# Optimization experiments

Hardware: AMD Instinct MI355X
Metric: run time of the kernel (lower is better)

Reference implementation:

```python
import jax, jax.numpy as jnp
import numpy as np

SCALING = 32.0 / 16.0  # alpha / rank


def setup_inputs() -> dict:
    key = jax.random.key(0)
    k1, k2, k3, k4, k5 = jax.random.split(key, 5)
    B_, S, D_in, D_out, R = 4, 2048, 4096, 4096, 16
    x = jax.random.normal(k1, (B_, S, D_in), dtype=jnp.float32)
    W = jax.random.normal(k2, (D_out, D_in), dtype=jnp.float32) * (1.0 / np.sqrt(D_in))
    b = jax.random.normal(k3, (D_out,), dtype=jnp.float32) * 0.02
    lora_A = jax.random.normal(k4, (R, D_in), dtype=jnp.float32) * (1.0 / np.sqrt(D_in))
    lora_B = jax.random.normal(k5, (D_out, R), dtype=jnp.float32) * 0.02
    return {"x": x, "W": W, "b": b, "lora_A": lora_A, "lora_B": lora_B}


def reference(x, W, b, lora_A, lora_B):
    # Base linear: y = x @ W^T + b
    base = jnp.einsum('bsd,od->bso', x, W) + b
    # LoRA path: ((x @ A^T) @ B^T) * scaling  (dropout=0 -> identity)
    xa = jnp.einsum('bsd,rd->bsr', x, lora_A)      # [B,S,r]
    lora = jnp.einsum('bsr,or->bso', xa, lora_B)    # [B,S,D_out]
    return base + lora * SCALING
```

## Files before the change

### kernel.cpp

```cpp
#include <hip/hip_runtime.h>
#include <hip/hip_bf16.h>
#include <stdint.h>

typedef __bf16 bf16x8 __attribute__((ext_vector_type(8)));
typedef float  f32x4  __attribute__((ext_vector_type(4)));
typedef unsigned short u16x8 __attribute__((ext_vector_type(8)));


__device__ __forceinline__ unsigned short f32_to_bf16_rne(float f) {
  union { float f; unsigned int u; } v; v.f = f;
  unsigned int u = v.u;
  unsigned int r = u + 0x7fffu + ((u >> 16) & 1u);
  return (unsigned short)(r >> 16);
}

__device__ __forceinline__ void async16(const unsigned short* g, unsigned short* l) {
  __builtin_amdgcn_global_load_lds(
      (const __attribute__((address_space(1))) unsigned int*)g,
      (__attribute__((address_space(3))) unsigned int*)l,
      16, 0, 0);
}

__global__ __launch_bounds__(256) void make_wp(const float* __restrict__ W,
                                               const float* __restrict__ lA,
                                               const float* __restrict__ lB,
                                               unsigned short* __restrict__ Wp) {
  const int o   = blockIdx.x;
  const int tid = threadIdx.x;
  __shared__ float sB[16];
  if (tid < 16) sB[tid] = lB[o * 16 + tid] * 2.0f;
  __syncthreads();
  #pragma unroll
  for (int it = 0; it < 4; ++it) {
    const int k = (it * 256 + tid) * 4;
    float4 acc = *(const float4*)(W + (size_t)o * 4096 + k);
    #pragma unroll
    for (int r = 0; r < 16; ++r) {
      const float4 a = *(const float4*)(lA + (size_t)r * 4096 + k);
      const float s = sB[r];
      acc.x += s * a.x; acc.y += s * a.y; acc.z += s * a.z; acc.w += s * a.w;
    }
    ushort4 ov;
    ov.x = f32_to_bf16_rne(acc.x);
    ov.y = f32_to_bf16_rne(acc.y);
    ov.z = f32_to_bf16_rne(acc.z);
    ov.w = f32_to_bf16_rne(acc.w);
    *(ushort4*)(Wp + (size_t)o * 4096 + k) = ov;
  }
}

__global__ __launch_bounds__(256) void cast_x(const float* __restrict__ x,
                                              unsigned short* __restrict__ xb,
                                              int n8) {
  const int idx = blockIdx.x * 256 + threadIdx.x;
  if (idx >= n8) return;
  const float4* p = (const float4*)x + (size_t)idx * 2;
  const float4 f0 = p[0], f1 = p[1];
  u16x8 o;
  o[0] = f32_to_bf16_rne(f0.x); o[1] = f32_to_bf16_rne(f0.y);
  o[2] = f32_to_bf16_rne(f0.z); o[3] = f32_to_bf16_rne(f0.w);
  o[4] = f32_to_bf16_rne(f1.x); o[5] = f32_to_bf16_rne(f1.y);
  o[6] = f32_to_bf16_rne(f1.z); o[7] = f32_to_bf16_rne(f1.w);
  *((u16x8*)xb + idx) = o;
}

#define BM 128
#define BN 128
#define BK 32
#define GEMM_M 8192
#define GEMM_N 4096
#define GEMM_K 4096

template <bool A_F32>
__global__ __launch_bounds__(256) void gemm_bias(
    const void* __restrict__ Aptr,
    const unsigned short* __restrict__ B,
    const float* __restrict__ bias,
    float* __restrict__ C) {
  __shared__ __align__(16) unsigned short sA[BM * BK];
  __shared__ __align__(16) unsigned short sB[BM * BK];

  const int tid  = threadIdx.x;
  const int wave = tid >> 6;
  const int lane = tid & 63;

  const int srow = tid >> 2;
  const int scol = (tid & 3) << 3;

  const size_t a_row0 = (size_t)blockIdx.y * BM;
  const size_t b_row0 = (size_t)blockIdx.x * BN;

  const unsigned short* bg0 = B + (b_row0 +      srow) * GEMM_K + scol;
  const unsigned short* bg1 = B + (b_row0 + 64 + srow) * GEMM_K + scol;

  unsigned short* sA0 = sA +        wave * 512;
  unsigned short* sA1 = sA + 2048 + wave * 512;
  unsigned short* sB0 = sB +        wave * 512;
  unsigned short* sB1 = sB + 2048 + wave * 512;

  const unsigned short* ag0 = nullptr; const unsigned short* ag1 = nullptr;
  const float* af0 = nullptr; const float* af1 = nullptr;
  if constexpr (A_F32) {
    af0 = (const float*)Aptr + (a_row0 +      srow) * GEMM_K + scol;
    af1 = (const float*)Aptr + (a_row0 + 64 + srow) * GEMM_K + scol;
  } else {
    ag0 = (const unsigned short*)Aptr + (a_row0 +      srow) * GEMM_K + scol;
    ag1 = (const unsigned short*)Aptr + (a_row0 + 64 + srow) * GEMM_K + scol;
  }
  unsigned short* sAw0 = sA +        tid * 8;
  unsigned short* sAw1 = sA + 2048 + tid * 8;

  const int wm   = (wave >> 1) * 64;
  const int wn   = (wave & 1) * 64;
  const int lrow = lane & 15;
  const int lk   = (lane >> 4) * 8;

  const unsigned short* sa_rd = sA + (wm + lrow) * BK + lk;
  const unsigned short* sb_rd = sB + (wn + lrow) * BK + lk;

  f32x4 acc[4][4];
  #pragma unroll
  for (int i = 0; i < 4; ++i)
    #pragma unroll
    for (int j = 0; j < 4; ++j)
      acc[i][j] = (f32x4){0.f, 0.f, 0.f, 0.f};

  for (int k0 = 0; k0 < GEMM_K; k0 += BK) {
    __syncthreads();
    async16(bg0 + k0, sB0);
    async16(bg1 + k0, sB1);
    if constexpr (A_F32) {
      const float* p0 = af0 + k0;
      const float* p1 = af1 + k0;
      const float4 x0 = *(const float4*)(p0);
      const float4 x1 = *(const float4*)(p0 + 4);
      const float4 y0 = *(const float4*)(p1);
      const float4 y1 = *(const float4*)(p1 + 4);
      u16x8 w0, w1;
      w0[0] = f32_to_bf16_rne(x0.x); w0[1] = f32_to_bf16_rne(x0.y);
      w0[2] = f32_to_bf16_rne(x0.z); w0[3] = f32_to_bf16_rne(x0.w);
      w0[4] = f32_to_bf16_rne(x1.x); w0[5] = f32_to_bf16_rne(x1.y);
      w0[6] = f32_to_bf16_rne(x1.z); w0[7] = f32_to_bf16_rne(x1.w);
      w1[0] = f32_to_bf16_rne(y0.x); w1[1] = f32_to_bf16_rne(y0.y);
      w1[2] = f32_to_bf16_rne(y0.z); w1[3] = f32_to_bf16_rne(y0.w);
      w1[4] = f32_to_bf16_rne(y1.x); w1[5] = f32_to_bf16_rne(y1.y);
      w1[6] = f32_to_bf16_rne(y1.z); w1[7] = f32_to_bf16_rne(y1.w);
      *(u16x8*)sAw0 = w0;
      *(u16x8*)sAw1 = w1;
    } else {
      async16(ag0 + k0, sA0);
      async16(ag1 + k0, sA1);
    }
    __syncthreads();

    bf16x8 af[4], bf[4];
    #pragma unroll
    for (int i = 0; i < 4; ++i) {
      af[i] = *(const bf16x8*)(sa_rd + i * 16 * BK);
      bf[i] = *(const bf16x8*)(sb_rd + i * 16 * BK);
    }
    #pragma unroll
    for (int i = 0; i < 4; ++i)
      #pragma unroll
      for (int j = 0; j < 4; ++j)
        acc[i][j] = __builtin_amdgcn_mfma_f32_16x16x32_bf16(af[i], bf[j], acc[i][j], 0, 0, 0);
  }

  const int row0 = (int)a_row0 + wm + (lane >> 4) * 4;
  const int col0 = (int)b_row0 + wn + lrow;
  float bv[4];
  #pragma unroll
  for (int j = 0; j < 4; ++j) bv[j] = bias[col0 + j * 16];
  #pragma unroll
  for (int i = 0; i < 4; ++i)
    #pragma unroll
    for (int j = 0; j < 4; ++j) {
      const int col = col0 + j * 16;
      #pragma unroll
      for (int r = 0; r < 4; ++r) {
        const int row = row0 + i * 16 + r;
        C[(size_t)row * GEMM_N + col] = acc[i][j][r] + bv[j];
      }
    }
}


extern "C" void kernel_launch(void* const* d_in, const int* in_sizes, int n_in,
                              void* d_out, int out_size, void* d_ws, size_t ws_size,
                              hipStream_t stream) {
  const float* x  = (const float*)d_in[0];
  const float* W  = (const float*)d_in[1];
  const float* b  = (const float*)d_in[2];
  const float* lA = (const float*)d_in[3];
  const float* lB = (const float*)d_in[4];
  float* out = (float*)d_out;
  (void)in_sizes; (void)n_in; (void)out_size;

  const size_t WP_BYTES = (size_t)4096 * 4096 * 2;
  const size_t XB_BYTES = (size_t)8192 * 4096 * 2;
  unsigned short* Wp = (unsigned short*)d_ws;

  make_wp<<<4096, 256, 0, stream>>>(W, lA, lB, Wp);

  if (ws_size >= WP_BYTES + XB_BYTES) {
    unsigned short* xb = Wp + (size_t)4096 * 4096;
    cast_x<<<(4194304 + 255) / 256, 256, 0, stream>>>(x, xb, 4194304);
    gemm_bias<false><<<dim3(GEMM_N / BN, GEMM_M / BM), 256, 0, stream>>>(
        (const void*)xb, Wp, b, out);
  } else {
    gemm_bias<true><<<dim3(GEMM_N / BN, GEMM_M / BM), 256, 0, stream>>>(
        (const void*)x, Wp, b, out);
  }
}
```

Baseline: 602.1 us.

## Fuse x bf16 cast into GEMM and reuse LoRA A across rows in make_wp

```diff
diff --git a/kernel.cpp b/kernel.cpp
--- a/kernel.cpp
+++ b/kernel.cpp
@@ -25,20 +25,23 @@
                                                const float* __restrict__ lA,
                                                const float* __restrict__ lB,
                                                unsigned short* __restrict__ Wp) {
-  const int o   = blockIdx.x;
-  const int tid = threadIdx.x;
-  __shared__ float sB[16];
-  if (tid < 16) sB[tid] = lB[o * 16 + tid] * 2.0f;
-  __syncthreads();
+  const int ro = (blockIdx.x & 511) * 8;
+  const int k  = (blockIdx.x >> 9) * 1024 + threadIdx.x * 4;
+
+  float4 a[16];
   #pragma unroll
-  for (int it = 0; it < 4; ++it) {
-    const int k = (it * 256 + tid) * 4;
+  for (int r = 0; r < 16; ++r)
+    a[r] = *(const float4*)(lA + (size_t)r * 4096 + k);
+
+  #pragma unroll
+  for (int i = 0; i < 8; ++i) {
+    const int o = ro + i;
     float4 acc = *(const float4*)(W + (size_t)o * 4096 + k);
     #pragma unroll
     for (int r = 0; r < 16; ++r) {
-      const float4 a = *(const float4*)(lA + (size_t)r * 4096 + k);
-      const float s = sB[r];
-      acc.x += s * a.x; acc.y += s * a.y; acc.z += s * a.z; acc.w += s * a.w;
+      const float s = lB[o * 16 + r] * 2.0f;
+      acc.x += s * a[r].x; acc.y += s * a[r].y;
+      acc.z += s * a[r].z; acc.w += s * a[r].w;
     }
     ushort4 ov;
     ov.x = f32_to_bf16_rne(acc.x);
@@ -49,21 +52,6 @@
   }
 }
 
-__global__ __launch_bounds__(256) void cast_x(const float* __restrict__ x,
-                                              unsigned short* __restrict__ xb,
-                                              int n8) {
-  const int idx = blockIdx.x * 256 + threadIdx.x;
-  if (idx >= n8) return;
-  const float4* p = (const float4*)x + (size_t)idx * 2;
-  const float4 f0 = p[0], f1 = p[1];
-  u16x8 o;
-  o[0] = f32_to_bf16_rne(f0.x); o[1] = f32_to_bf16_rne(f0.y);
-  o[2] = f32_to_bf16_rne(f0.z); o[3] = f32_to_bf16_rne(f0.w);
-  o[4] = f32_to_bf16_rne(f1.x); o[5] = f32_to_bf16_rne(f1.y);
-  o[6] = f32_to_bf16_rne(f1.z); o[7] = f32_to_bf16_rne(f1.w);
-  *((u16x8*)xb + idx) = o;
-}
-
 #define BM 128
 #define BN 128
 #define BK 32
@@ -71,9 +59,8 @@
 #define GEMM_N 4096
 #define GEMM_K 4096
 
-template <bool A_F32>
 __global__ __launch_bounds__(256) void gemm_bias(
-    const void* __restrict__ Aptr,
+    const float* __restrict__ A,
     const unsigned short* __restrict__ B,
     const float* __restrict__ bias,
     float* __restrict__ C) {
@@ -92,21 +79,11 @@
 
   const unsigned short* bg0 = B + (b_row0 +      srow) * GEMM_K + scol;
   const unsigned short* bg1 = B + (b_row0 + 64 + srow) * GEMM_K + scol;
+  const float*          af0 = A + (a_row0 +      srow) * GEMM_K + scol;
+  const float*          af1 = A + (a_row0 + 64 + srow) * GEMM_K + scol;
 
-  unsigned short* sA0 = sA +        wave * 512;
-  unsigned short* sA1 = sA + 2048 + wave * 512;
   unsigned short* sB0 = sB +        wave * 512;
   unsigned short* sB1 = sB + 2048 + wave * 512;
-
-  const unsigned short* ag0 = nullptr; const unsigned short* ag1 = nullptr;
-  const float* af0 = nullptr; const float* af1 = nullptr;
-  if constexpr (A_F32) {
-    af0 = (const float*)Aptr + (a_row0 +      srow) * GEMM_K + scol;
-    af1 = (const float*)Aptr + (a_row0 + 64 + srow) * GEMM_K + scol;
-  } else {
-    ag0 = (const unsigned short*)Aptr + (a_row0 +      srow) * GEMM_K + scol;
-    ag1 = (const unsigned short*)Aptr + (a_row0 + 64 + srow) * GEMM_K + scol;
-  }
   unsigned short* sAw0 = sA +        tid * 8;
   unsigned short* sAw1 = sA + 2048 + tid * 8;
 
@@ -129,7 +106,7 @@
     __syncthreads();
     async16(bg0 + k0, sB0);
     async16(bg1 + k0, sB1);
-    if constexpr (A_F32) {
+    {
       const float* p0 = af0 + k0;
       const float* p1 = af1 + k0;
       const float4 x0 = *(const float4*)(p0);
@@ -147,9 +124,6 @@
       w1[6] = f32_to_bf16_rne(y1.z); w1[7] = f32_to_bf16_rne(y1.w);
       *(u16x8*)sAw0 = w0;
       *(u16x8*)sAw1 = w1;
-    } else {
-      async16(ag0 + k0, sA0);
-      async16(ag1 + k0, sA1);
     }
     __syncthreads();
 
@@ -194,21 +168,10 @@
   const float* lA = (const float*)d_in[3];
   const float* lB = (const float*)d_in[4];
   float* out = (float*)d_out;
-  (void)in_sizes; (void)n_in; (void)out_size;
+  (void)in_sizes; (void)n_in; (void)out_size; (void)ws_size;
 
-  const size_t WP_BYTES = (size_t)4096 * 4096 * 2;
-  const size_t XB_BYTES = (size_t)8192 * 4096 * 2;
   unsigned short* Wp = (unsigned short*)d_ws;
 
-  make_wp<<<4096, 256, 0, stream>>>(W, lA, lB, Wp);
-
-  if (ws_size >= WP_BYTES + XB_BYTES) {
-    unsigned short* xb = Wp + (size_t)4096 * 4096;
-    cast_x<<<(4194304 + 255) / 256, 256, 0, stream>>>(x, xb, 4194304);
-    gemm_bias<false><<<dim3(GEMM_N / BN, GEMM_M / BM), 256, 0, stream>>>(
-        (const void*)xb, Wp, b, out);
-  } else {
-    gemm_bias<true><<<dim3(GEMM_N / BN, GEMM_M / BM), 256, 0, stream>>>(
-        (const void*)x, Wp, b, out);
-  }
+  make_wp<<<2048, 256, 0, stream>>>(W, lA, lB, Wp);
+  gemm_bias<<<dim3(GEMM_N / BN, GEMM_M / BM), 256, 0, stream>>>(x, Wp, b, out);
 }
```

Result: slower. 708.8 us (+17.7%).
